# Kernel optimization log

Hardware: AMD Instinct MI355X
Metric: run time of the kernel (lower is better)

The kernel has to match this reference:

```python
import jax, jax.numpy as jnp
import numpy as np

B, D, E, H, C, TOPK = 4096, 768, 16, 768, 1000, 4

def setup_inputs() -> dict:
    key = jax.random.key(0)
    ks = jax.random.split(key, 4)
    s_in = 1.0 / np.sqrt(D)
    return {
        'features': jax.random.normal(ks[0], (B, D), dtype=jnp.float32),
        'router_w': jax.random.normal(ks[1], (D, E), dtype=jnp.float32) * s_in,
        'router_b': jnp.zeros((E,), jnp.float32),
        'ln_g': jnp.ones((E, D), jnp.float32),
        'ln_b': jnp.zeros((E, D), jnp.float32),
        'w1': jax.random.normal(ks[2], (E, D, H), dtype=jnp.float32) * s_in,
        'b1': jnp.zeros((E, H), jnp.float32),
        'w2': jax.random.normal(ks[3], (E, H, C), dtype=jnp.float32) * (1.0 / np.sqrt(H)),
        'b2': jnp.zeros((E, C), jnp.float32),
    }

def reference(features, router_w, router_b, ln_g, ln_b, w1, b1, w2, b2):
    # router
    gate_logits = features @ router_w + router_b          # [B,E]
    gate_probs = jax.nn.softmax(gate_logits, axis=-1)
    topk_vals, topk_idx = jax.lax.top_k(gate_probs, TOPK)  # [B,K]
    topk_vals = topk_vals / jnp.sum(topk_vals, axis=-1, keepdims=True)

    # all experts computed densely: LayerNorm (per-expert affine) -> Linear -> GELU -> Linear
    mu = jnp.mean(features, axis=-1, keepdims=True)
    var = jnp.mean((features - mu) ** 2, axis=-1, keepdims=True)
    xn = (features - mu) / jnp.sqrt(var + 1e-5)            # [B,D]
    y = xn[:, None, :] * ln_g[None, :, :] + ln_b[None, :, :]  # [B,E,D]
    h = jax.nn.gelu(jnp.einsum('bed,edh->beh', y, w1) + b1[None], approximate=False)  # [B,E,H]
    all_logits = jnp.einsum('beh,ehc->bec', h, w2) + b2[None]  # [B,E,C]

    # top-k gather + weighted softmax mixture
    selected = jnp.take_along_axis(all_logits, topk_idx[:, :, None], axis=1)  # [B,K,C]
    market_probs = jnp.sum(topk_vals[:, :, None] * jax.nn.softmax(selected, axis=-1), axis=1)  # [B,C]
    all_probs = jax.nn.softmax(jnp.transpose(all_logits, (1, 0, 2)), axis=-1)  # [E,B,C]
    return market_probs, all_probs, gate_probs
```

## Files before the change

kernel.cpp:

```cpp
#include <hip/hip_runtime.h>
#include <hip/hip_bf16.h>
#include <cmath>

#define B_ 4096
#define D_ 768
#define E_ 16
#define H_ 768
#define C_ 1000
#define CP_ 1024
#define K_ 768

typedef __bf16 bf16_t;
typedef __bf16 bf16x8 __attribute__((ext_vector_type(8)));
typedef float f32x4 __attribute__((ext_vector_type(4)));

__device__ __forceinline__ void async_lds16(const void* g, void* l) {
  __builtin_amdgcn_global_load_lds(
      (const __attribute__((address_space(1))) void*)g,
      (__attribute__((address_space(3))) void*)l, 16, 0, 0);
}

__global__ __launch_bounds__(256) void k_router_ln(
    const float* __restrict__ feat, const float* __restrict__ rw,
    const float* __restrict__ rb, float* __restrict__ gate_out,
    int* __restrict__ tk_idx, float* __restrict__ tk_val,
    bf16_t* __restrict__ xn) {
  int w = threadIdx.x >> 6, lane = threadIdx.x & 63;
  int b = blockIdx.x * 4 + w;
  float acc[E_];
#pragma unroll
  for (int e = 0; e < E_; ++e) acc[e] = 0.f;
  const float* frow = feat + (size_t)b * D_;
  float v[D_ / 64];
  float s = 0.f, sq = 0.f;
#pragma unroll
  for (int it = 0; it < D_ / 64; ++it) {
    int d = it * 64 + lane;
    float f = frow[d];
    v[it] = f; s += f; sq += f * f;
    const float4* r4 = reinterpret_cast<const float4*>(rw + (size_t)d * E_);
    float4 q0 = r4[0], q1 = r4[1], q2 = r4[2], q3 = r4[3];
    acc[0]  += f * q0.x; acc[1]  += f * q0.y; acc[2]  += f * q0.z; acc[3]  += f * q0.w;
    acc[4]  += f * q1.x; acc[5]  += f * q1.y; acc[6]  += f * q1.z; acc[7]  += f * q1.w;
    acc[8]  += f * q2.x; acc[9]  += f * q2.y; acc[10] += f * q2.z; acc[11] += f * q2.w;
    acc[12] += f * q3.x; acc[13] += f * q3.y; acc[14] += f * q3.z; acc[15] += f * q3.w;
  }
#pragma unroll
  for (int off = 32; off; off >>= 1) { s += __shfl_xor(s, off); sq += __shfl_xor(sq, off); }
  float mu = s * (1.f / D_);
  float var = sq * (1.f / D_) - mu * mu;
  float rs = rsqrtf(var + 1e-5f);
  bf16_t* o = xn + (size_t)b * D_;
#pragma unroll
  for (int it = 0; it < D_ / 64; ++it)
    o[it * 64 + lane] = (bf16_t)((v[it] - mu) * rs);
#pragma unroll
  for (int e = 0; e < E_; ++e) {
#pragma unroll
    for (int off = 32; off; off >>= 1) acc[e] += __shfl_xor(acc[e], off);
    acc[e] += rb[e];
  }
  if (lane == 0) {
    float mx = acc[0];
#pragma unroll
    for (int e = 1; e < E_; ++e) mx = fmaxf(mx, acc[e]);
    float p[E_]; float ps = 0.f;
#pragma unroll
    for (int e = 0; e < E_; ++e) { p[e] = expf(acc[e] - mx); ps += p[e]; }
    float inv = 1.f / ps;
    float* go = gate_out + (size_t)b * E_;
#pragma unroll
    for (int e = 0; e < E_; ++e) { p[e] *= inv; go[e] = p[e]; }
    float lg[E_];
#pragma unroll
    for (int e = 0; e < E_; ++e) lg[e] = acc[e];
    int idx4[4]; float v4[4]; float vs = 0.f;
#pragma unroll
    for (int k = 0; k < 4; ++k) {
      int bi = 0; float bv = -1e30f;
#pragma unroll
      for (int e = 0; e < E_; ++e) { if (lg[e] > bv) { bv = lg[e]; bi = e; } }
      idx4[k] = bi; v4[k] = p[bi]; vs += p[bi]; lg[bi] = -1e30f;
    }
    float nv = 1.f / vs;
#pragma unroll
    for (int k = 0; k < 4; ++k) { tk_idx[b * 4 + k] = idx4[k]; tk_val[b * 4 + k] = v4[k] * nv; }
  }
}

__global__ void k_tw1b(const float* __restrict__ w1, const float* __restrict__ lng,
                       const float* __restrict__ lnb, const float* __restrict__ b1,
                       bf16_t* __restrict__ w1T, float* __restrict__ bias1) {
  __shared__ float t[32][33];
  __shared__ float br[8][33];
  int hT = blockIdx.x * 32, e = blockIdx.y;
  int tx = threadIdx.x, ty = threadIdx.y;
  const float* w1e = w1 + (size_t)e * D_ * H_;
  const float* ge = lng + (size_t)e * D_;
  const float* lb = lnb + (size_t)e * D_;
  bf16_t* o = w1T + (size_t)e * H_ * D_;
  float bsum = 0.f;
  for (int r0 = 0; r0 < D_ / 32; ++r0) {
#pragma unroll
    for (int s = 0; s < 4; ++s) {
      int dl = ty + s * 8;
      int d = r0 * 32 + dl;
      float val = w1e[(size_t)d * H_ + hT + tx];
      t[dl][tx] = val * ge[d];
      bsum += lb[d] * val;
    }
    __syncthreads();
#pragma unroll
    for (int s = 0; s < 4; ++s) {
      int hl = ty + s * 8;
      o[(size_t)(hT + hl) * D_ + r0 * 32 + tx] = (bf16_t)t[tx][hl];
    }
    __syncthreads();
  }
  br[ty][tx] = bsum;
  __syncthreads();
  if (ty == 0) {
    float a = 0.f;
#pragma unroll
    for (int z = 0; z < 8; ++z) a += br[z][tx];
    bias1[(size_t)e * H_ + hT + tx] = b1[(size_t)e * H_ + hT + tx] + a;
  }
}

__global__ void k_tw2(const float* __restrict__ w2, bf16_t* __restrict__ w2T) {
  __shared__ float t[32][33];
  int e = blockIdx.z, hT = blockIdx.y * 32, cT = blockIdx.x * 32;
  int tx = threadIdx.x, ty = threadIdx.y;
  const float* w2e = w2 + (size_t)e * H_ * C_;
#pragma unroll
  for (int r = 0; r < 4; ++r) {
    int h = hT + ty + r * 8, c = cT + tx;
    t[ty + r * 8][tx] = (c < C_) ? w2e[(size_t)h * C_ + c] : 0.f;
  }
  __syncthreads();
  bf16_t* o = w2T + (size_t)e * CP_ * H_;
#pragma unroll
  for (int r = 0; r < 4; ++r) {
    int c = cT + ty + r * 8;
    o[(size_t)c * H_ + hT + tx] = (bf16_t)t[tx][ty + r * 8];
  }
}

template <int MODE>
__global__ __launch_bounds__(512, 2) void k_gemm256(
    const bf16_t* __restrict__ Abase, size_t aStride,
    const bf16_t* __restrict__ Bt, int Np,
    const float* __restrict__ bias,
    bf16_t* __restrict__ outb, float* __restrict__ outf) {
  __shared__ __attribute__((aligned(16))) bf16_t smbuf[2][2][256 * 64];
  int id = blockIdx.x;
  int xcd = id & 7, seq = id >> 3;
  int e, m0, n0;
  if (MODE == 0) {
    int m = seq / 6, rr = seq % 6;
    e = xcd * 2 + rr / 3;
    m0 = m * 256;
    n0 = (rr % 3) * 256;
  } else {
    e = xcd * 2 + (seq >> 6);
    int rr = seq & 63;
    m0 = (rr >> 2) * 256;
    n0 = (rr & 3) * 256;
  }
  const bf16_t* A = Abase + (size_t)e * aStride + (size_t)m0 * K_;
  const bf16_t* Bp = Bt + ((size_t)e * Np + n0) * K_;

  int tid = threadIdx.x;
  int lane = tid & 63;
  int wid = tid >> 6;
  int wm = wid >> 2, wn = wid & 3;
  int fr = lane & 15, hi = lane >> 4;
  int sw0 = (hi ^ (fr & 7)) * 8;

  int srow = tid >> 3;
  int scg = (tid & 7) ^ (srow & 7);
  const bf16_t* asrc = A + (size_t)srow * K_ + scg * 8;
  const bf16_t* bsrc = Bp + (size_t)srow * K_ + scg * 8;

  f32x4 acc[8][4];
#pragma unroll
  for (int i = 0; i < 8; ++i)
#pragma unroll
    for (int j = 0; j < 4; ++j) acc[i][j] = f32x4{0.f, 0.f, 0.f, 0.f};

  auto STAGE = [&](int kt, int nb) {
    bf16_t* ad = &smbuf[nb][0][tid * 8];
    bf16_t* bd = &smbuf[nb][1][tid * 8];
    const bf16_t* as = asrc + kt * 64;
    const bf16_t* bs = bsrc + kt * 64;
#pragma unroll
    for (int s = 0; s < 4; ++s) {
      async_lds16(as + (size_t)s * 64 * K_, ad + s * 4096);
      async_lds16(bs + (size_t)s * 64 * K_, bd + s * 4096);
    }
  };

  bf16x8 af[4][2], bfr[2][2];
  auto COMPUTE = [&](int cur) {
    const bf16_t* Ala = &smbuf[cur][0][(wm * 128 + fr) * 64];
    const bf16_t* Bla = &smbuf[cur][1][(wn * 64 + fr) * 64];
#pragma unroll
    for (int q = 0; q < 4; ++q) {
      const int mq = q >> 1;
      const int nq = (q == 1 || q == 2);
      if (q == 0 || q == 2) {
#pragma unroll
        for (int i = 0; i < 4; ++i)
#pragma unroll
          for (int ks = 0; ks < 2; ++ks)
            af[i][ks] = *(const bf16x8*)&Ala[(mq * 64 + i * 16) * 64 + (sw0 ^ (ks * 32))];
      }
      if (q != 2) {
#pragma unroll
        for (int j = 0; j < 2; ++j)
#pragma unroll
          for (int ks = 0; ks < 2; ++ks)
            bfr[j][ks] = *(const bf16x8*)&Bla[(nq * 32 + j * 16) * 64 + (sw0 ^ (ks * 32))];
      }
      __builtin_amdgcn_s_barrier();
      __builtin_amdgcn_s_setprio(1);
#pragma unroll
      for (int i = 0; i < 4; ++i)
#pragma unroll
        for (int j = 0; j < 2; ++j)
#pragma unroll
          for (int ks = 0; ks < 2; ++ks)
            acc[mq * 4 + i][nq * 2 + j] = __builtin_amdgcn_mfma_f32_16x16x32_bf16(
                af[i][ks], bfr[j][ks], acc[mq * 4 + i][nq * 2 + j], 0, 0, 0);
      __builtin_amdgcn_s_setprio(0);
      __builtin_amdgcn_s_barrier();
    }
  };

  constexpr int NKT = K_ / 64;
  STAGE(0, 0);
  for (int t = 0; t < NKT - 1; ++t) {
    STAGE(t + 1, (t + 1) & 1);
    asm volatile("s_waitcnt vmcnt(8)" ::: "memory");
    __builtin_amdgcn_s_barrier();
    COMPUTE(t & 1);
  }
  asm volatile("s_waitcnt vmcnt(0)" ::: "memory");
  __builtin_amdgcn_s_barrier();
  COMPUTE((NKT - 1) & 1);

  int rb = hi * 4;
  int cl = fr;
#pragma unroll
  for (int i = 0; i < 8; ++i) {
#pragma unroll
    for (int j = 0; j < 4; ++j) {
      int n = n0 + wn * 64 + j * 16 + cl;
      if (MODE == 0) {
        float bs = bias[(size_t)e * H_ + n];
#pragma unroll
        for (int r = 0; r < 4; ++r) {
          int m = m0 + wm * 128 + i * 16 + rb + r;
          float vv = acc[i][j][r] + bs;
          vv = 0.5f * vv * (1.f + erff(vv * 0.70710678118654752f));
          outb[((size_t)e * B_ + m) * H_ + n] = (bf16_t)vv;
        }
      } else if (MODE == 1) {
        float bs = (n < C_) ? bias[(size_t)e * C_ + n] : 0.f;
#pragma unroll
        for (int r = 0; r < 4; ++r) {
          int m = m0 + wm * 128 + i * 16 + rb + r;
          outb[((size_t)e * B_ + m) * CP_ + n] = (bf16_t)(acc[i][j][r] + bs);
        }
      } else {
        if (n < C_) {
          float bs = bias[(size_t)e * C_ + n];
#pragma unroll
          for (int r = 0; r < 4; ++r) {
            int m = m0 + wm * 128 + i * 16 + rb + r;
            outf[((size_t)e * B_ + m) * C_ + n] = acc[i][j][r] + bs;
          }
        }
      }
    }
  }
}

__global__ __launch_bounds__(256) void k_sm_market(
    const bf16_t* __restrict__ lg, const int* __restrict__ tki,
    const float* __restrict__ tkv, float* __restrict__ out1,
    float* __restrict__ out0) {
  int w = threadIdx.x >> 6, lane = threadIdx.x & 63;
  int b = blockIdx.x * 4 + w;
  const int* ixp = tki + (size_t)b * 4;
  const float* vvp = tkv + (size_t)b * 4;
  int i0 = ixp[0], i1 = ixp[1], i2 = ixp[2], i3 = ixp[3];
  float v0 = vvp[0], v1 = vvp[1], v2 = vvp[2], v3 = vvp[3];
  float mac[2][8];
#pragma unroll
  for (int it = 0; it < 2; ++it)
#pragma unroll
    for (int q = 0; q < 8; ++q) mac[it][q] = 0.f;
#pragma unroll 2
  for (int e = 0; e < E_; ++e) {
    const bf16_t* row = lg + ((size_t)e * B_ + b) * CP_;
    float f[2][8];
    float mx = -1e30f;
#pragma unroll
    for (int it = 0; it < 2; ++it) {
      int ch = it * 64 + lane;
      bf16x8 x = *(const bf16x8*)(row + ch * 8);
      if (ch < 125) {
#pragma unroll
        for (int q = 0; q < 8; ++q) { f[it][q] = (float)x[q]; mx = fmaxf(mx, f[it][q]); }
      }
    }
#pragma unroll
    for (int off = 32; off; off >>= 1) mx = fmaxf(mx, __shfl_xor(mx, off));
    float s = 0.f;
#pragma unroll
    for (int it = 0; it < 2; ++it) {
      int ch = it * 64 + lane;
      if (ch < 125) {
#pragma unroll
        for (int q = 0; q < 8; ++q) { f[it][q] = __expf(f[it][q] - mx); s += f[it][q]; }
      }
    }
#pragma unroll
    for (int off = 32; off; off >>= 1) s += __shfl_xor(s, off);
    float inv = 1.f / s;
    float wg = (i0 == e ? v0 : 0.f) + (i1 == e ? v1 : 0.f) +
               (i2 == e ? v2 : 0.f) + (i3 == e ? v3 : 0.f);
    float* orow = out1 + ((size_t)e * B_ + b) * C_;
#pragma unroll
    for (int it = 0; it < 2; ++it) {
      int ch = it * 64 + lane;
      if (ch < 125) {
        float p[8];
#pragma unroll
        for (int q = 0; q < 8; ++q) { p[q] = f[it][q] * inv; mac[it][q] += wg * p[q]; }
        *(float4*)(orow + ch * 8)     = make_float4(p[0], p[1], p[2], p[3]);
        *(float4*)(orow + ch * 8 + 4) = make_float4(p[4], p[5], p[6], p[7]);
      }
    }
  }
  float* mrow = out0 + (size_t)b * C_;
#pragma unroll
  for (int it = 0; it < 2; ++it) {
    int ch = it * 64 + lane;
    if (ch < 125) {
      *(float4*)(mrow + ch * 8)     = make_float4(mac[it][0], mac[it][1], mac[it][2], mac[it][3]);
      *(float4*)(mrow + ch * 8 + 4) = make_float4(mac[it][4], mac[it][5], mac[it][6], mac[it][7]);
    }
  }
}

__global__ __launch_bounds__(256) void k_softmax(float* __restrict__ p) {
  int w = threadIdx.x >> 6, lane = threadIdx.x & 63;
  size_t r = (size_t)blockIdx.x * 4 + w;
  float* row = p + r * C_;
  float4* row4 = reinterpret_cast<float4*>(row);
  const int n4 = C_ / 4;
  float4 v[4];
  float mx = -1e30f;
#pragma unroll
  for (int i = 0; i < 4; ++i) {
    int idx = i * 64 + lane;
    if (idx < n4) {
      v[i] = row4[idx];
      mx = fmaxf(mx, fmaxf(fmaxf(v[i].x, v[i].y), fmaxf(v[i].z, v[i].w)));
    }
  }
#pragma unroll
  for (int off = 32; off; off >>= 1) mx = fmaxf(mx, __shfl_xor(mx, off));
  float s = 0.f;
#pragma unroll
  for (int i = 0; i < 4; ++i) {
    int idx = i * 64 + lane;
    if (idx < n4) {
      v[i].x = __expf(v[i].x - mx); v[i].y = __expf(v[i].y - mx);
      v[i].z = __expf(v[i].z - mx); v[i].w = __expf(v[i].w - mx);
      s += v[i].x + v[i].y + v[i].z + v[i].w;
    }
  }
#pragma unroll
  for (int off = 32; off; off >>= 1) s += __shfl_xor(s, off);
  float inv = 1.f / s;
#pragma unroll
  for (int i = 0; i < 4; ++i) {
    int idx = i * 64 + lane;
    if (idx < n4) {
      v[i].x *= inv; v[i].y *= inv; v[i].z *= inv; v[i].w *= inv;
      row4[idx] = v[i];
    }
  }
}

__global__ __launch_bounds__(256) void k_market(const float* __restrict__ allp,
                                                const int* __restrict__ tki,
                                                const float* __restrict__ tkv,
                                                float* __restrict__ out0) {
  int b = blockIdx.y;
  int c = blockIdx.x * 256 + threadIdx.x;
  if (c >= C_) return;
  const int* ix = tki + (size_t)b * 4;
  const float* vv = tkv + (size_t)b * 4;
  float s = 0.f;
#pragma unroll
  for (int k = 0; k < 4; ++k)
    s += vv[k] * allp[((size_t)ix[k] * B_ + b) * C_ + c];
  out0[(size_t)b * C_ + c] = s;
}

extern "C" void kernel_launch(void* const* d_in, const int* in_sizes, int n_in,
                              void* d_out, int out_size, void* d_ws, size_t ws_size,
                              hipStream_t stream) {
  const float* feat = (const float*)d_in[0];
  const float* rw   = (const float*)d_in[1];
  const float* rb   = (const float*)d_in[2];
  const float* lng  = (const float*)d_in[3];
  const float* lnb  = (const float*)d_in[4];
  const float* w1   = (const float*)d_in[5];
  const float* b1   = (const float*)d_in[6];
  const float* w2   = (const float*)d_in[7];
  const float* b2   = (const float*)d_in[8];

  float* out0 = (float*)d_out;
  float* out1 = out0 + (size_t)B_ * C_;
  float* out2 = out1 + (size_t)E_ * B_ * C_;

  char* ws = (char*)d_ws;
  size_t off = 0;
  auto take = [&](size_t bytes) -> void* {
    void* p = ws + off;
    off += (bytes + 255) & ~(size_t)255;
    return p;
  };
  bf16_t* xn   = (bf16_t*)take((size_t)B_ * D_ * 2);
  bf16_t* w1T  = (bf16_t*)take((size_t)E_ * H_ * D_ * 2);
  bf16_t* w2T  = (bf16_t*)take((size_t)E_ * CP_ * H_ * 2);
  float* bias1 = (float*)take((size_t)E_ * H_ * 4);
  int* tki     = (int*)take((size_t)B_ * 4 * 4);
  float* tkv   = (float*)take((size_t)B_ * 4 * 4);
  bf16_t* Hact = (bf16_t*)take((size_t)E_ * B_ * H_ * 2);
  size_t logit_bytes = (size_t)E_ * B_ * CP_ * 2;
  bool use_b16_logits = (off + logit_bytes) <= ws_size;
  bf16_t* logitsB = use_b16_logits ? (bf16_t*)take(logit_bytes) : nullptr;

  k_router_ln<<<B_ / 4, 256, 0, stream>>>(feat, rw, rb, out2, tki, tkv, xn);
  k_tw1b<<<dim3(24, E_), dim3(32, 8), 0, stream>>>(w1, lng, lnb, b1, w1T, bias1);
  k_tw2<<<dim3(32, 24, E_), dim3(32, 8), 0, stream>>>(w2, w2T);
  k_gemm256<0><<<E_ * 16 * 3, 512, 0, stream>>>(xn, 0, w1T, H_, bias1, Hact, nullptr);
  if (use_b16_logits) {
    k_gemm256<1><<<E_ * 16 * 4, 512, 0, stream>>>(Hact, (size_t)B_ * H_, w2T, CP_, b2, logitsB, nullptr);
    k_sm_market<<<B_ / 4, 256, 0, stream>>>(logitsB, tki, tkv, out1, out0);
  } else {
    k_gemm256<2><<<E_ * 16 * 4, 512, 0, stream>>>(Hact, (size_t)B_ * H_, w2T, CP_, b2, nullptr, out1);
    k_softmax<<<(E_ * B_) / 4, 256, 0, stream>>>(out1);
    k_market<<<dim3(4, B_), 256, 0, stream>>>(out1, tki, tkv, out0);
  }
}
```

Baseline: 708.9 us.

## Parallelize w1 transpose over D tiles and use polynomial GELU approximation

The w1 transpose/fold kernel previously ran only 24x16 blocks, each looping over all of D. It now launches a 3D grid that also tiles D and accumulates the LN-bias contribution with atomicAdd into a bias buffer pre-initialized by a new small kernel. Separately, the exact erf-based GELU in the first GEMM epilogue is replaced by an Abramowitz-Stegun style polynomial CDF approximation using rcp and exp, which is cheaper but slightly less accurate and makes bias sums order-nondeterministic.

```diff
diff --git a/kernel.cpp b/kernel.cpp
--- a/kernel.cpp
+++ b/kernel.cpp
@@ -18,6 +18,17 @@
   __builtin_amdgcn_global_load_lds(
       (const __attribute__((address_space(1))) void*)g,
       (__attribute__((address_space(3))) void*)l, 16, 0, 0);
+}
+
+__device__ __forceinline__ float gelu_f(float x) {
+  float ax = fabsf(x);
+  float t = __builtin_amdgcn_rcpf(fmaf(0.2316419f, ax, 1.0f));
+  float p = t * fmaf(t, fmaf(t, fmaf(t, fmaf(t, 1.330274429f, -1.821255978f),
+                                     1.781477937f), -0.356563782f), 0.319381530f);
+  float phi = 0.3989422804f * __expf(-0.5f * ax * ax);
+  float q = phi * p;
+  float cdf = (x >= 0.f) ? (1.f - q) : q;
+  return x * cdf;
 }
 
 __global__ __launch_bounds__(256) void k_router_ln(
@@ -88,42 +99,43 @@
   }
 }
 
-__global__ void k_tw1b(const float* __restrict__ w1, const float* __restrict__ lng,
-                       const float* __restrict__ lnb, const float* __restrict__ b1,
-                       bf16_t* __restrict__ w1T, float* __restrict__ bias1) {
+__global__ __launch_bounds__(256) void k_bias_init(const float* __restrict__ b1,
+                                                   float* __restrict__ bias1) {
+  int i = blockIdx.x * 256 + threadIdx.x;
+  bias1[i] = b1[i];
+}
+
+__global__ void k_tw1(const float* __restrict__ w1, const float* __restrict__ lng,
+                      const float* __restrict__ lnb, bf16_t* __restrict__ w1T,
+                      float* __restrict__ bias1) {
   __shared__ float t[32][33];
   __shared__ float br[8][33];
-  int hT = blockIdx.x * 32, e = blockIdx.y;
+  int e = blockIdx.z, dT = blockIdx.y * 32, hT = blockIdx.x * 32;
   int tx = threadIdx.x, ty = threadIdx.y;
   const float* w1e = w1 + (size_t)e * D_ * H_;
   const float* ge = lng + (size_t)e * D_;
   const float* lb = lnb + (size_t)e * D_;
-  bf16_t* o = w1T + (size_t)e * H_ * D_;
   float bsum = 0.f;
-  for (int r0 = 0; r0 < D_ / 32; ++r0) {
-#pragma unroll
-    for (int s = 0; s < 4; ++s) {
-      int dl = ty + s * 8;
-      int d = r0 * 32 + dl;
-      float val = w1e[(size_t)d * H_ + hT + tx];
-      t[dl][tx] = val * ge[d];
-      bsum += lb[d] * val;
-    }
-    __syncthreads();
-#pragma unroll
-    for (int s = 0; s < 4; ++s) {
-      int hl = ty + s * 8;
-      o[(size_t)(hT + hl) * D_ + r0 * 32 + tx] = (bf16_t)t[tx][hl];
-    }
-    __syncthreads();
+#pragma unroll
+  for (int r = 0; r < 4; ++r) {
+    int d = dT + ty + r * 8;
+    float val = w1e[(size_t)d * H_ + hT + tx];
+    t[ty + r * 8][tx] = val * ge[d];
+    bsum += lb[d] * val;
   }
   br[ty][tx] = bsum;
   __syncthreads();
+  bf16_t* o = w1T + (size_t)e * H_ * D_;
+#pragma unroll
+  for (int r = 0; r < 4; ++r) {
+    int h = hT + ty + r * 8;
+    o[(size_t)h * D_ + dT + tx] = (bf16_t)t[tx][ty + r * 8];
+  }
   if (ty == 0) {
     float a = 0.f;
 #pragma unroll
     for (int z = 0; z < 8; ++z) a += br[z][tx];
-    bias1[(size_t)e * H_ + hT + tx] = b1[(size_t)e * H_ + hT + tx] + a;
+    atomicAdd(&bias1[(size_t)e * H_ + hT + tx], a);
   }
 }
 
@@ -262,8 +274,7 @@
         for (int r = 0; r < 4; ++r) {
           int m = m0 + wm * 128 + i * 16 + rb + r;
           float vv = acc[i][j][r] + bs;
-          vv = 0.5f * vv * (1.f + erff(vv * 0.70710678118654752f));
-          outb[((size_t)e * B_ + m) * H_ + n] = (bf16_t)vv;
+          outb[((size_t)e * B_ + m) * H_ + n] = (bf16_t)gelu_f(vv);
         }
       } else if (MODE == 1) {
         float bs = (n < C_) ? bias[(size_t)e * C_ + n] : 0.f;
@@ -448,7 +459,8 @@
   bf16_t* logitsB = use_b16_logits ? (bf16_t*)take(logit_bytes) : nullptr;
 
   k_router_ln<<<B_ / 4, 256, 0, stream>>>(feat, rw, rb, out2, tki, tkv, xn);
-  k_tw1b<<<dim3(24, E_), dim3(32, 8), 0, stream>>>(w1, lng, lnb, b1, w1T, bias1);
+  k_bias_init<<<E_ * H_ / 256, 256, 0, stream>>>(b1, bias1);
+  k_tw1<<<dim3(24, 24, E_), dim3(32, 8), 0, stream>>>(w1, lng, lnb, w1T, bias1);
   k_tw2<<<dim3(32, 24, E_), dim3(32, 8), 0, stream>>>(w2, w2T);
   k_gemm256<0><<<E_ * 16 * 3, 512, 0, stream>>>(xn, 0, w1T, H_, bias1, Hact, nullptr);
   if (use_b16_logits) {
```

After: 665.0 us. 6.2% less time.
